# Performance work log

Hardware: AMD Instinct MI355X
Metric: run time of the kernel (lower is better)

The kernel has to match this reference:

```python
import jax, jax.numpy as jnp
import numpy as np


def setup_inputs() -> dict:
    key = jax.random.key(0)
    k1, k2 = jax.random.split(key)
    H, D, N = 1, 256, 65536        # (heads=1, embedding_dim, num_tokens)
    C = 1024                       # num_embeddings (codebook size)
    inputs = jax.random.normal(k1, (H, D, N), dtype=jnp.float32)
    embedding = jax.random.normal(k2, (H, C, D), dtype=jnp.float32)
    return {"inputs": inputs, "embedding": embedding}


COMMITMENT_COST = 0.25


def reference(inputs, embedding):
    # inputs: (h, d, n) -> flat: (h, n, d)
    flat = jnp.transpose(inputs, (0, 2, 1))
    # negative euclidean distance (matches -torch.cdist, p=2)
    x2 = jnp.sum(flat * flat, axis=-1, keepdims=True)            # (h, n, 1)
    e2 = jnp.sum(embedding * embedding, axis=-1)[:, None, :]     # (h, 1, c)
    xe = jnp.einsum('hnd,hcd->hnc', flat, embedding)             # (h, n, c)
    d2 = jnp.maximum(x2 + e2 - 2.0 * xe, 0.0)
    distances = -jnp.sqrt(d2)                                    # (h, n, c)
    encoding_indices = jnp.argmax(distances, axis=2)             # (h, n)
    # gather codebook vectors: h == 1
    quantized = jnp.take(embedding[0], encoding_indices[0], axis=0)[None]  # (h, n, d)
    commit_loss = jnp.mean((jax.lax.stop_gradient(quantized) - flat) ** 2)
    loss = COMMITMENT_COST * commit_loss
    # straight-through estimator
    quantized_st = flat + jax.lax.stop_gradient(quantized - flat)
    out = jnp.transpose(quantized_st, (0, 2, 1))                 # (h, d, n)
    return out, encoding_indices, loss, distances
```

## Files before the change

### kernel.cpp

```cpp
#include <hip/hip_runtime.h>
#include <math.h>

#define N_TOK 65536
#define D_DIM 256
#define C_NUM 1024

#define OUT_OFF   0
#define IDX_OFF   (D_DIM * N_TOK)
#define LOSS_OFF  (IDX_OFF + N_TOK)
#define DIST_OFF  (LOSS_OFF + 1)

#define EH_OFF_F  0
#define EL_OFF_F  131072
#define E2_OFF_F  262144
#define PART_OFF_F 263168
#define NPART 4096

typedef __attribute__((ext_vector_type(8))) short bf16x8;
typedef __attribute__((ext_vector_type(4))) float f32x4;

static __device__ __forceinline__ unsigned short f2bf(float f) {
  unsigned int u = __float_as_uint(f);
  unsigned int r = (u + 0x7fffu + ((u >> 16) & 1u)) >> 16;
  return (unsigned short)r;
}
static __device__ __forceinline__ float bf2f(unsigned short h) {
  return __uint_as_float(((unsigned int)h) << 16);
}

__global__ __launch_bounds__(256) void kA_prep(const float* __restrict__ X,
                                               const float* __restrict__ E,
                                               float* __restrict__ out) {
  const int bid = blockIdx.x, tid = threadIdx.x;
  if (bid < 256) {
    const int n = bid * 256 + tid;
    float s = 0.0f;
#pragma unroll 8
    for (int d = 0; d < D_DIM; ++d) {
      float v = X[(size_t)d * N_TOK + n];
      s = fmaf(v, v, s);
    }
    out[IDX_OFF + n] = s;
  } else {
    unsigned short* EhG = (unsigned short*)(out + EH_OFF_F);
    unsigned short* ElG = (unsigned short*)(out + EL_OFF_F);
    const int lane = tid & 63, w = tid >> 6;
#pragma unroll 1
    for (int cc = 0; cc < 16; ++cc) {
      const int c = (bid - 256) * 64 + w * 16 + cc;
      const float4 v = *(const float4*)(E + (size_t)c * D_DIM + lane * 4);
      unsigned short h0 = f2bf(v.x), h1 = f2bf(v.y), h2 = f2bf(v.z), h3 = f2bf(v.w);
      unsigned short l0 = f2bf(v.x - bf2f(h0)), l1 = f2bf(v.y - bf2f(h1));
      unsigned short l2 = f2bf(v.z - bf2f(h2)), l3 = f2bf(v.w - bf2f(h3));
      ushort4 hv = make_ushort4(h0, h1, h2, h3);
      ushort4 lv = make_ushort4(l0, l1, l2, l3);
      *(ushort4*)(EhG + (size_t)c * D_DIM + lane * 4) = hv;
      *(ushort4*)(ElG + (size_t)c * D_DIM + lane * 4) = lv;
      float s = v.x * v.x + v.y * v.y + v.z * v.z + v.w * v.w;
#pragma unroll
      for (int off = 32; off; off >>= 1) s += __shfl_down(s, off, 64);
      if (lane == 0) out[E2_OFF_F + c] = s;
    }
  }
}

#define TM 64
#define TC 256
#define BK 32
#define XS 40

__global__ __launch_bounds__(256) void k2_dist(const float* __restrict__ X,
                                               float* __restrict__ out) {
  __shared__ __align__(16) unsigned short xh[2][TM * XS];
  __shared__ __align__(16) unsigned short xl[2][TM * XS];

  const unsigned short* __restrict__ EhG = (const unsigned short*)(out + EH_OFF_F);
  const unsigned short* __restrict__ ElG = (const unsigned short*)(out + EL_OFF_F);

  const int tid = threadIdx.x;
  const int lane = tid & 63, wave = tid >> 6;

  const int bid = blockIdx.x;
  const int xcd = bid & 7;
  const int slot = bid >> 3;
  const int bx = slot & 3;
  const int by = xcd * 128 + (slot >> 2);
  const int c0 = bx * TC;
  const int n0 = by * TM;

  const int wc = c0 + wave * 64;
  const int m = lane & 15;
  const int q = lane >> 4;

  f32x4 acc[4][4];
#pragma unroll
  for (int i = 0; i < 4; ++i)
#pragma unroll
    for (int t = 0; t < 4; ++t) acc[i][t] = (f32x4){0.f, 0.f, 0.f, 0.f};

  const int sn = lane;
  const int kg = wave;

  float xv[8];
  {
    const float* xp = X + (size_t)(kg * 8) * N_TOK + n0 + sn;
#pragma unroll
    for (int j = 0; j < 8; ++j) xv[j] = xp[(size_t)j * N_TOK];
  }

#pragma unroll 1
  for (int kb = 0; kb < D_DIM; kb += BK) {
    const int p = (kb >> 5) & 1;

    bf16x8 bh[4], bl[4];
#pragma unroll
    for (int t = 0; t < 4; ++t) {
      const size_t eoff = (size_t)(wc + t * 16 + m) * D_DIM + kb + q * 8;
      bh[t] = *(const bf16x8*)(EhG + eoff);
      bl[t] = *(const bf16x8*)(ElG + eoff);
    }

    unsigned short hh[8], ll[8];
#pragma unroll
    for (int j = 0; j < 8; ++j) {
      hh[j] = f2bf(xv[j]);
      ll[j] = f2bf(xv[j] - bf2f(hh[j]));
    }
    *(bf16x8*)&xh[p][sn * XS + kg * 8] = *(bf16x8*)hh;
    *(bf16x8*)&xl[p][sn * XS + kg * 8] = *(bf16x8*)ll;

    if (kb + BK < D_DIM) {
      const float* xp = X + (size_t)(kb + BK + kg * 8) * N_TOK + n0 + sn;
#pragma unroll
      for (int j = 0; j < 8; ++j) xv[j] = xp[(size_t)j * N_TOK];
    }

    __syncthreads();

    bf16x8 ah[4], al[4];
#pragma unroll
    for (int i = 0; i < 4; ++i) {
      const int ro = (i * 16 + m) * XS + q * 8;
      ah[i] = *(const bf16x8*)&xh[p][ro];
      al[i] = *(const bf16x8*)&xl[p][ro];
    }
#pragma unroll
    for (int i = 0; i < 4; ++i)
#pragma unroll
      for (int t = 0; t < 4; ++t) {
        acc[i][t] = __builtin_amdgcn_mfma_f32_16x16x32_bf16(ah[i], bh[t], acc[i][t], 0, 0, 0);
        acc[i][t] = __builtin_amdgcn_mfma_f32_16x16x32_bf16(ah[i], bl[t], acc[i][t], 0, 0, 0);
        acc[i][t] = __builtin_amdgcn_mfma_f32_16x16x32_bf16(al[i], bh[t], acc[i][t], 0, 0, 0);
      }
  }

  float e2v[4];
#pragma unroll
  for (int t = 0; t < 4; ++t) e2v[t] = out[E2_OFF_F + wc + t * 16 + m];

#pragma unroll
  for (int i = 0; i < 4; ++i) {
#pragma unroll
    for (int r = 0; r < 4; ++r) {
      const int tok = n0 + i * 16 + q * 4 + r;
      const float x2v = out[IDX_OFF + tok];
      const size_t row = DIST_OFF + (size_t)tok * C_NUM;
#pragma unroll
      for (int t = 0; t < 4; ++t) {
        float d2 = fmaf(-2.0f, acc[i][t][r], x2v + e2v[t]);
        d2 = fmaxf(d2, 0.0f);
        out[row + wc + t * 16 + m] = -sqrtf(d2);
      }
    }
  }
}

#define MARGIN 0.01f

__global__ __launch_bounds__(256) void k3_argmax(const float* __restrict__ X,
                                                 const float* __restrict__ E,
                                                 float* __restrict__ out) {
  __shared__ float lsum[4];
  const int tid = threadIdx.x, lane = tid & 63, w = tid >> 6;
  float wloss = 0.0f;

#pragma unroll 1
  for (int it = 0; it < 4; ++it) {
    const int n = blockIdx.x * 16 + w * 4 + it;
    const float* row = out + DIST_OFF + (size_t)n * C_NUM;

    float v[16];
    float best = -3.4e38f;
    int bi = 0x7fffffff;
#pragma unroll
    for (int j = 0; j < 16; ++j) {
      v[j] = row[j * 64 + lane];
      if (v[j] > best) { best = v[j]; bi = j * 64 + lane; }
    }
#pragma unroll
    for (int off = 32; off; off >>= 1) {
      const float ov = __shfl_xor(best, off, 64);
      const int oi = __shfl_xor(bi, off, 64);
      if (ov > best || (ov == best && oi < bi)) { best = ov; bi = oi; }
    }
    const float thr = best - MARGIN;
    unsigned long long masks[16];
    int total = 0;
#pragma unroll
    for (int j = 0; j < 16; ++j) {
      masks[j] = __ballot(v[j] > thr);
      total += __popcll(masks[j]);
    }
    float best_d2 = best * best;
    int best_idx = bi;
    if (total > 1) {
      best_d2 = 3.4e38f;
      best_idx = 0x7fffffff;
      for (int j = 0; j < 16; ++j) {
        unsigned long long mm = masks[j];
        while (mm) {
          const int l = __ffsll((long long)mm) - 1;
          mm &= mm - 1;
          const int c = j * 64 + l;
          float sx = 0.f, se = 0.f, sxe = 0.f;
#pragma unroll
          for (int r = 0; r < 4; ++r) {
            const int d = r * 64 + lane;
            const float xv = X[(size_t)d * N_TOK + n];
            const float ev = E[(size_t)c * D_DIM + d];
            sx = fmaf(xv, xv, sx);
            se = fmaf(ev, ev, se);
            sxe = fmaf(xv, ev, sxe);
          }
          float d2 = fmaf(-2.f, sxe, sx + se);
#pragma unroll
          for (int off = 32; off; off >>= 1) d2 += __shfl_xor(d2, off, 64);
          d2 = fmaxf(d2, 0.f);
          if (d2 < best_d2 || (d2 == best_d2 && c < best_idx)) {
            best_d2 = d2; best_idx = c;
          }
        }
      }
    }
    if (lane == 0) out[IDX_OFF + n] = (float)best_idx;
    wloss += best_d2;
  }
  if (lane == 0) lsum[w] = wloss;
  __syncthreads();
  if (tid == 0)
    out[PART_OFF_F + blockIdx.x] = lsum[0] + lsum[1] + lsum[2] + lsum[3];
}

__global__ __launch_bounds__(256) void k3b_loss(float* __restrict__ out) {
  __shared__ float red[4];
  const int tid = threadIdx.x, lane = tid & 63, w = tid >> 6;
  float s = 0.0f;
#pragma unroll
  for (int i = 0; i < NPART / 256; ++i) s += out[PART_OFF_F + i * 256 + tid];
#pragma unroll
  for (int off = 32; off; off >>= 1) s += __shfl_down(s, off, 64);
  if (lane == 0) red[w] = s;
  __syncthreads();
  if (tid == 0)
    out[LOSS_OFF] = (red[0] + red[1] + red[2] + red[3]) *
                    (0.25f / ((float)N_TOK * (float)D_DIM));
}

__global__ __launch_bounds__(256) void k4_gather(const float* __restrict__ E,
                                                 float* __restrict__ out) {
  const int g = blockIdx.x * 256 + threadIdx.x;
  const int n = g * 4;
  const int i0 = (int)out[IDX_OFF + n + 0];
  const int i1 = (int)out[IDX_OFF + n + 1];
  const int i2 = (int)out[IDX_OFF + n + 2];
  const int i3 = (int)out[IDX_OFF + n + 3];
  const float* e0 = E + (size_t)i0 * D_DIM;
  const float* e1 = E + (size_t)i1 * D_DIM;
  const float* e2 = E + (size_t)i2 * D_DIM;
  const float* e3 = E + (size_t)i3 * D_DIM;
  const int d0 = blockIdx.y * 32;
#pragma unroll 4
  for (int d = d0; d < d0 + 32; ++d) {
    float4 wv = make_float4(e0[d], e1[d], e2[d], e3[d]);
    *(float4*)&out[(size_t)d * N_TOK + n] = wv;
  }
}

extern "C" void kernel_launch(void* const* d_in, const int* in_sizes, int n_in,
                              void* d_out, int out_size, void* d_ws, size_t ws_size,
                              hipStream_t stream) {
  const float* X = (const float*)d_in[0];
  const float* E = (const float*)d_in[1];
  float* out = (float*)d_out;

  hipLaunchKernelGGL(kA_prep, dim3(272), dim3(256), 0, stream, X, E, out);
  hipLaunchKernelGGL(k2_dist, dim3((C_NUM / TC) * (N_TOK / TM)), dim3(256), 0,
                     stream, X, out);
  hipLaunchKernelGGL(k3_argmax, dim3(N_TOK / 16), dim3(256), 0, stream, X, E, out);
  hipLaunchKernelGGL(k3b_loss, dim3(1), dim3(256), 0, stream, out);
  hipLaunchKernelGGL(k4_gather, dim3(N_TOK / 4 / 256, 8), dim3(256), 0, stream,
                     E, out);
}
```

Measured before the change: 618.8 us.

## Pre-split X into token-major bf16 hi/lo arrays and drop LDS staging in distance GEMM

A new prep kernel converts the whole input into token-major bf16 hi/lo arrays, stored in the out buffer's scratch region, and moves the codebook hi/lo split and norms into the workspace. The distance kernel then loads both operands straight from global memory into MFMA fragments, with no shared-memory staging or barriers. This removes the per-tile conversion and the __syncthreads stall. In exchange it writes and re-reads about 64MB of bf16 intermediate data, and the fragment loads are strided 16-byte reads that may cache less well. The old path is kept as a fallback when no workspace is available.

```diff
diff --git a/kernel.cpp b/kernel.cpp
--- a/kernel.cpp
+++ b/kernel.cpp
@@ -10,10 +10,7 @@
 #define LOSS_OFF  (IDX_OFF + N_TOK)
 #define DIST_OFF  (LOSS_OFF + 1)
 
-#define EH_OFF_F  0
-#define EL_OFF_F  131072
-#define E2_OFF_F  262144
-#define PART_OFF_F 263168
+#define MARGIN 0.01f
 #define NPART 4096
 
 typedef __attribute__((ext_vector_type(8))) short bf16x8;
@@ -27,6 +24,255 @@
 static __device__ __forceinline__ float bf2f(unsigned short h) {
   return __uint_as_float(((unsigned int)h) << 16);
 }
+
+
+#define WS_EH   0
+#define WS_EL   524288
+#define WS_E2   1048576
+#define WS_NEEDED (WS_E2 + 4096)
+
+#define XH_OFF_F 0
+#define XL_OFF_F 8388608
+
+#define PART_OFF_F 263168
+
+__global__ __launch_bounds__(256) void kA2_prep(const float* __restrict__ X,
+                                                const float* __restrict__ E,
+                                                float* __restrict__ out,
+                                                unsigned char* __restrict__ ws) {
+  const int bid = blockIdx.x, tid = threadIdx.x;
+  if (bid < 1024) {
+    unsigned short* XhG = (unsigned short*)(out + XH_OFF_F);
+    unsigned short* XlG = (unsigned short*)(out + XL_OFF_F);
+    const int n = bid * 64 + (tid >> 2);
+    const int sg = (tid & 3) * 16;
+    unsigned short* xh = XhG + (size_t)n * D_DIM;
+    unsigned short* xl = XlG + (size_t)n * D_DIM;
+#pragma unroll 1
+    for (int dc = 0; dc < D_DIM; dc += 64) {
+      float v[16];
+#pragma unroll
+      for (int j = 0; j < 16; ++j) v[j] = X[(size_t)(dc + sg + j) * N_TOK + n];
+      unsigned short hh[16], ll[16];
+#pragma unroll
+      for (int j = 0; j < 16; ++j) {
+        hh[j] = f2bf(v[j]);
+        ll[j] = f2bf(v[j] - bf2f(hh[j]));
+      }
+      *(bf16x8*)(xh + dc + sg) = *(bf16x8*)&hh[0];
+      *(bf16x8*)(xh + dc + sg + 8) = *(bf16x8*)&hh[8];
+      *(bf16x8*)(xl + dc + sg) = *(bf16x8*)&ll[0];
+      *(bf16x8*)(xl + dc + sg + 8) = *(bf16x8*)&ll[8];
+    }
+  } else if (bid < 1040) {
+    unsigned short* EhG = (unsigned short*)(ws + WS_EH);
+    unsigned short* ElG = (unsigned short*)(ws + WS_EL);
+    float* e2p = (float*)(ws + WS_E2);
+    const int lane = tid & 63, w = tid >> 6;
+#pragma unroll 1
+    for (int cc = 0; cc < 16; ++cc) {
+      const int c = (bid - 1024) * 64 + w * 16 + cc;
+      const float4 v = *(const float4*)(E + (size_t)c * D_DIM + lane * 4);
+      unsigned short h0 = f2bf(v.x), h1 = f2bf(v.y), h2 = f2bf(v.z), h3 = f2bf(v.w);
+      unsigned short l0 = f2bf(v.x - bf2f(h0)), l1 = f2bf(v.y - bf2f(h1));
+      unsigned short l2 = f2bf(v.z - bf2f(h2)), l3 = f2bf(v.w - bf2f(h3));
+      ushort4 hv = make_ushort4(h0, h1, h2, h3);
+      ushort4 lv = make_ushort4(l0, l1, l2, l3);
+      *(ushort4*)(EhG + (size_t)c * D_DIM + lane * 4) = hv;
+      *(ushort4*)(ElG + (size_t)c * D_DIM + lane * 4) = lv;
+      float s = v.x * v.x + v.y * v.y + v.z * v.z + v.w * v.w;
+#pragma unroll
+      for (int off = 32; off; off >>= 1) s += __shfl_down(s, off, 64);
+      if (lane == 0) e2p[c] = s;
+    }
+  } else {
+    const int n = (bid - 1040) * 256 + tid;
+    float s = 0.0f;
+#pragma unroll 8
+    for (int d = 0; d < D_DIM; ++d) {
+      float v = X[(size_t)d * N_TOK + n];
+      s = fmaf(v, v, s);
+    }
+    out[IDX_OFF + n] = s;
+  }
+}
+
+#define TM 64
+#define TC 256
+#define BK 32
+
+__global__ __launch_bounds__(256) void k2b_dist(float* __restrict__ out,
+                                                unsigned char* __restrict__ ws) {
+  const unsigned short* __restrict__ XhG = (const unsigned short*)(out + XH_OFF_F);
+  const unsigned short* __restrict__ EhG = (const unsigned short*)(ws + WS_EH);
+  const float* __restrict__ e2p = (const float*)(ws + WS_E2);
+
+  const int tid = threadIdx.x;
+  const int lane = tid & 63, wave = tid >> 6;
+
+  const int bid = blockIdx.x;
+  const int xcd = bid & 7;
+  const int slot = bid >> 3;
+  const int bx = slot & 3;
+  const int by = xcd * 128 + (slot >> 2);
+  const int c0 = bx * TC;
+  const int n0 = by * TM;
+
+  const int wc = c0 + wave * 64;
+  const int m = lane & 15;
+  const int q = lane >> 4;
+
+  f32x4 acc[4][4];
+#pragma unroll
+  for (int i = 0; i < 4; ++i)
+#pragma unroll
+    for (int t = 0; t < 4; ++t) acc[i][t] = (f32x4){0.f, 0.f, 0.f, 0.f};
+
+  const unsigned short* ap[4];
+  const unsigned short* bp[4];
+#pragma unroll
+  for (int i = 0; i < 4; ++i) ap[i] = XhG + (size_t)(n0 + i * 16 + m) * D_DIM + q * 8;
+#pragma unroll
+  for (int t = 0; t < 4; ++t) bp[t] = EhG + (size_t)(wc + t * 16 + m) * D_DIM + q * 8;
+  const size_t loDu = (size_t)(XL_OFF_F - XH_OFF_F) * 2;
+  const size_t loEu = (size_t)(WS_EL - WS_EH) / 2;
+
+#pragma unroll 2
+  for (int kb = 0; kb < D_DIM; kb += BK) {
+    bf16x8 ah[4], al[4], bh[4], bl[4];
+#pragma unroll
+    for (int t = 0; t < 4; ++t) {
+      bh[t] = *(const bf16x8*)(bp[t] + kb);
+      bl[t] = *(const bf16x8*)(bp[t] + loEu + kb);
+    }
+#pragma unroll
+    for (int i = 0; i < 4; ++i) {
+      ah[i] = *(const bf16x8*)(ap[i] + kb);
+      al[i] = *(const bf16x8*)(ap[i] + loDu + kb);
+    }
+#pragma unroll
+    for (int i = 0; i < 4; ++i)
+#pragma unroll
+      for (int t = 0; t < 4; ++t) {
+        acc[i][t] = __builtin_amdgcn_mfma_f32_16x16x32_bf16(ah[i], bh[t], acc[i][t], 0, 0, 0);
+        acc[i][t] = __builtin_amdgcn_mfma_f32_16x16x32_bf16(ah[i], bl[t], acc[i][t], 0, 0, 0);
+        acc[i][t] = __builtin_amdgcn_mfma_f32_16x16x32_bf16(al[i], bh[t], acc[i][t], 0, 0, 0);
+      }
+  }
+
+  float e2v[4];
+#pragma unroll
+  for (int t = 0; t < 4; ++t) e2v[t] = e2p[wc + t * 16 + m];
+
+#pragma unroll
+  for (int i = 0; i < 4; ++i) {
+#pragma unroll
+    for (int r = 0; r < 4; ++r) {
+      const int tok = n0 + i * 16 + q * 4 + r;
+      const float x2v = out[IDX_OFF + tok];
+      const size_t row = DIST_OFF + (size_t)tok * C_NUM;
+#pragma unroll
+      for (int t = 0; t < 4; ++t) {
+        float d2 = fmaf(-2.0f, acc[i][t][r], x2v + e2v[t]);
+        d2 = fmaxf(d2, 0.0f);
+        out[row + wc + t * 16 + m] = -sqrtf(d2);
+      }
+    }
+  }
+}
+
+__global__ __launch_bounds__(256) void k3_argmax(const float* __restrict__ X,
+                                                 const float* __restrict__ E,
+                                                 float* __restrict__ out) {
+  __shared__ float lsum[4];
+  const int tid = threadIdx.x, lane = tid & 63, w = tid >> 6;
+  float wloss = 0.0f;
+
+#pragma unroll 1
+  for (int it = 0; it < 4; ++it) {
+    const int n = blockIdx.x * 16 + w * 4 + it;
+    const float* row = out + DIST_OFF + (size_t)n * C_NUM;
+
+    float v[16];
+    float best = -3.4e38f;
+    int bi = 0x7fffffff;
+#pragma unroll
+    for (int j = 0; j < 16; ++j) {
+      v[j] = row[j * 64 + lane];
+      if (v[j] > best) { best = v[j]; bi = j * 64 + lane; }
+    }
+#pragma unroll
+    for (int off = 32; off; off >>= 1) {
+      const float ov = __shfl_xor(best, off, 64);
+      const int oi = __shfl_xor(bi, off, 64);
+      if (ov > best || (ov == best && oi < bi)) { best = ov; bi = oi; }
+    }
+    const float thr = best - MARGIN;
+    unsigned long long masks[16];
+    int total = 0;
+#pragma unroll
+    for (int j = 0; j < 16; ++j) {
+      masks[j] = __ballot(v[j] > thr);
+      total += __popcll(masks[j]);
+    }
+    float best_d2 = best * best;
+    int best_idx = bi;
+    if (total > 1) {
+      best_d2 = 3.4e38f;
+      best_idx = 0x7fffffff;
+      for (int j = 0; j < 16; ++j) {
+        unsigned long long mm = masks[j];
+        while (mm) {
+          const int l = __ffsll((long long)mm) - 1;
+          mm &= mm - 1;
+          const int c = j * 64 + l;
+          float sx = 0.f, se = 0.f, sxe = 0.f;
+#pragma unroll
+          for (int r = 0; r < 4; ++r) {
+            const int d = r * 64 + lane;
+            const float xv = X[(size_t)d * N_TOK + n];
+            const float ev = E[(size_t)c * D_DIM + d];
+            sx = fmaf(xv, xv, sx);
+            se = fmaf(ev, ev, se);
+            sxe = fmaf(xv, ev, sxe);
+          }
+          float d2 = fmaf(-2.f, sxe, sx + se);
+#pragma unroll
+          for (int off = 32; off; off >>= 1) d2 += __shfl_xor(d2, off, 64);
+          d2 = fmaxf(d2, 0.f);
+          if (d2 < best_d2 || (d2 == best_d2 && c < best_idx)) {
+            best_d2 = d2; best_idx = c;
+          }
+        }
+      }
+    }
+    if (lane == 0) out[IDX_OFF + n] = (float)best_idx;
+    wloss += best_d2;
+  }
+  if (lane == 0) lsum[w] = wloss;
+  __syncthreads();
+  if (tid == 0)
+    out[PART_OFF_F + blockIdx.x] = lsum[0] + lsum[1] + lsum[2] + lsum[3];
+}
+
+__global__ __launch_bounds__(256) void k3b_loss(float* __restrict__ out) {
+  __shared__ float red[4];
+  const int tid = threadIdx.x, lane = tid & 63, w = tid >> 6;
+  float s = 0.0f;
+#pragma unroll
+  for (int i = 0; i < NPART / 256; ++i) s += out[PART_OFF_F + i * 256 + tid];
+#pragma unroll
+  for (int off = 32; off; off >>= 1) s += __shfl_down(s, off, 64);
+  if (lane == 0) red[w] = s;
+  __syncthreads();
+  if (tid == 0)
+    out[LOSS_OFF] = (red[0] + red[1] + red[2] + red[3]) *
+                    (0.25f / ((float)N_TOK * (float)D_DIM));
+}
+
+#define EH_OFF_F  0
+#define EL_OFF_F  131072
+#define E2_OFF_F  262144
 
 __global__ __launch_bounds__(256) void kA_prep(const float* __restrict__ X,
                                                const float* __restrict__ E,
@@ -64,9 +310,6 @@
   }
 }
 
-#define TM 64
-#define TC 256
-#define BK 32
 #define XS 40
 
 __global__ __launch_bounds__(256) void k2_dist(const float* __restrict__ X,
@@ -79,7 +322,6 @@
 
   const int tid = threadIdx.x;
   const int lane = tid & 63, wave = tid >> 6;
-
   const int bid = blockIdx.x;
   const int xcd = bid & 7;
   const int slot = bid >> 3;
@@ -111,7 +353,6 @@
 #pragma unroll 1
   for (int kb = 0; kb < D_DIM; kb += BK) {
     const int p = (kb >> 5) & 1;
-
     bf16x8 bh[4], bl[4];
 #pragma unroll
     for (int t = 0; t < 4; ++t) {
@@ -119,7 +360,6 @@
       bh[t] = *(const bf16x8*)(EhG + eoff);
       bl[t] = *(const bf16x8*)(ElG + eoff);
     }
-
     unsigned short hh[8], ll[8];
 #pragma unroll
     for (int j = 0; j < 8; ++j) {
@@ -128,15 +368,12 @@
     }
     *(bf16x8*)&xh[p][sn * XS + kg * 8] = *(bf16x8*)hh;
     *(bf16x8*)&xl[p][sn * XS + kg * 8] = *(bf16x8*)ll;
-
     if (kb + BK < D_DIM) {
       const float* xp = X + (size_t)(kb + BK + kg * 8) * N_TOK + n0 + sn;
 #pragma unroll
       for (int j = 0; j < 8; ++j) xv[j] = xp[(size_t)j * N_TOK];
     }
-
     __syncthreads();
-
     bf16x8 ah[4], al[4];
 #pragma unroll
     for (int i = 0; i < 4; ++i) {
@@ -173,97 +410,6 @@
       }
     }
   }
-}
-
-#define MARGIN 0.01f
-
-__global__ __launch_bounds__(256) void k3_argmax(const float* __restrict__ X,
-                                                 const float* __restrict__ E,
-                                                 float* __restrict__ out) {
-  __shared__ float lsum[4];
-  const int tid = threadIdx.x, lane = tid & 63, w = tid >> 6;
-  float wloss = 0.0f;
-
-#pragma unroll 1
-  for (int it = 0; it < 4; ++it) {
-    const int n = blockIdx.x * 16 + w * 4 + it;
-    const float* row = out + DIST_OFF + (size_t)n * C_NUM;
-
-    float v[16];
-    float best = -3.4e38f;
-    int bi = 0x7fffffff;
-#pragma unroll
-    for (int j = 0; j < 16; ++j) {
-      v[j] = row[j * 64 + lane];
-      if (v[j] > best) { best = v[j]; bi = j * 64 + lane; }
-    }
-#pragma unroll
-    for (int off = 32; off; off >>= 1) {
-      const float ov = __shfl_xor(best, off, 64);
-      const int oi = __shfl_xor(bi, off, 64);
-      if (ov > best || (ov == best && oi < bi)) { best = ov; bi = oi; }
-    }
-    const float thr = best - MARGIN;
-    unsigned long long masks[16];
-    int total = 0;
-#pragma unroll
-    for (int j = 0; j < 16; ++j) {
-      masks[j] = __ballot(v[j] > thr);
-      total += __popcll(masks[j]);
-    }
-    float best_d2 = best * best;
-    int best_idx = bi;
-    if (total > 1) {
-      best_d2 = 3.4e38f;
-      best_idx = 0x7fffffff;
-      for (int j = 0; j < 16; ++j) {
-        unsigned long long mm = masks[j];
-        while (mm) {
-          const int l = __ffsll((long long)mm) - 1;
-          mm &= mm - 1;
-          const int c = j * 64 + l;
-          float sx = 0.f, se = 0.f, sxe = 0.f;
-#pragma unroll
-          for (int r = 0; r < 4; ++r) {
-            const int d = r * 64 + lane;
-            const float xv = X[(size_t)d * N_TOK + n];
-            const float ev = E[(size_t)c * D_DIM + d];
-            sx = fmaf(xv, xv, sx);
-            se = fmaf(ev, ev, se);
-            sxe = fmaf(xv, ev, sxe);
-          }
-          float d2 = fmaf(-2.f, sxe, sx + se);
-#pragma unroll
-          for (int off = 32; off; off >>= 1) d2 += __shfl_xor(d2, off, 64);
-          d2 = fmaxf(d2, 0.f);
-          if (d2 < best_d2 || (d2 == best_d2 && c < best_idx)) {
-            best_d2 = d2; best_idx = c;
-          }
-        }
-      }
-    }
-    if (lane == 0) out[IDX_OFF + n] = (float)best_idx;
-    wloss += best_d2;
-  }
-  if (lane == 0) lsum[w] = wloss;
-  __syncthreads();
-  if (tid == 0)
-    out[PART_OFF_F + blockIdx.x] = lsum[0] + lsum[1] + lsum[2] + lsum[3];
-}
-
-__global__ __launch_bounds__(256) void k3b_loss(float* __restrict__ out) {
-  __shared__ float red[4];
-  const int tid = threadIdx.x, lane = tid & 63, w = tid >> 6;
-  float s = 0.0f;
-#pragma unroll
-  for (int i = 0; i < NPART / 256; ++i) s += out[PART_OFF_F + i * 256 + tid];
-#pragma unroll
-  for (int off = 32; off; off >>= 1) s += __shfl_down(s, off, 64);
-  if (lane == 0) red[w] = s;
-  __syncthreads();
-  if (tid == 0)
-    out[LOSS_OFF] = (red[0] + red[1] + red[2] + red[3]) *
-                    (0.25f / ((float)N_TOK * (float)D_DIM));
 }
 
 __global__ __launch_bounds__(256) void k4_gather(const float* __restrict__ E,
@@ -293,11 +439,22 @@
   const float* E = (const float*)d_in[1];
   float* out = (float*)d_out;
 
-  hipLaunchKernelGGL(kA_prep, dim3(272), dim3(256), 0, stream, X, E, out);
-  hipLaunchKernelGGL(k2_dist, dim3((C_NUM / TC) * (N_TOK / TM)), dim3(256), 0,
-                     stream, X, out);
-  hipLaunchKernelGGL(k3_argmax, dim3(N_TOK / 16), dim3(256), 0, stream, X, E, out);
-  hipLaunchKernelGGL(k3b_loss, dim3(1), dim3(256), 0, stream, out);
-  hipLaunchKernelGGL(k4_gather, dim3(N_TOK / 4 / 256, 8), dim3(256), 0, stream,
-                     E, out);
-}
+  if (ws_size >= WS_NEEDED && d_ws != nullptr) {
+    unsigned char* ws = (unsigned char*)d_ws;
+    hipLaunchKernelGGL(kA2_prep, dim3(1296), dim3(256), 0, stream, X, E, out, ws);
+    hipLaunchKernelGGL(k2b_dist, dim3((C_NUM / TC) * (N_TOK / TM)), dim3(256), 0,
+                       stream, out, ws);
+    hipLaunchKernelGGL(k3_argmax, dim3(N_TOK / 16), dim3(256), 0, stream, X, E, out);
+    hipLaunchKernelGGL(k3b_loss, dim3(1), dim3(256), 0, stream, out);
+    hipLaunchKernelGGL(k4_gather, dim3(N_TOK / 4 / 256, 8), dim3(256), 0, stream,
+                       E, out);
+  } else {
+    hipLaunchKernelGGL(kA_prep, dim3(272), dim3(256), 0, stream, X, E, out);
+    hipLaunchKernelGGL(k2_dist, dim3((C_NUM / TC) * (N_TOK / TM)), dim3(256), 0,
+                       stream, X, out);
+    hipLaunchKernelGGL(k3_argmax, dim3(N_TOK / 16), dim3(256), 0, stream, X, E, out);
+    hipLaunchKernelGGL(k3b_loss, dim3(1), dim3(256), 0, stream, out);
+    hipLaunchKernelGGL(k4_gather, dim3(N_TOK / 4 / 256, 8), dim3(256), 0, stream,
+                       E, out);
+  }
+}
```

Result: slower. 750.6 us (+21.3%).
